# Kernel tuning notes

Measured on AMD Instinct MI355X. Metric: run time of the kernel, lower is better.

## Reference

```python
import jax, jax.numpy as jnp
import numpy as np

B, LX, LY, D = 8, 2048, 2048, 256

def setup_inputs() -> dict:
    key = jax.random.key(0)
    k1, k2, k3, k4 = jax.random.split(key, 4)
    x = jax.random.normal(k1, (B, LX, D), dtype=jnp.float32)
    y = jax.random.normal(k2, (B, LY, D), dtype=jnp.float32)
    y_mask = jax.random.randint(k3, (B, LY), 0, 2).astype(jnp.bool_)
    W = jax.random.normal(k4, (D, D), dtype=jnp.float32) * (1.0 / np.sqrt(D))
    b = jnp.zeros((D,), dtype=jnp.float32)
    return {"x": x, "y": y, "y_mask": y_mask, "W": W, "b": b}

def reference(x, y, y_mask, W, b):
    # shared linear + relu projection (torch Linear: x @ W.T + b)
    x_proj = jax.nn.relu(jnp.einsum('bld,ed->ble', x, W) + b)  # [B,LX,D]
    y_proj = jax.nn.relu(jnp.einsum('bld,ed->ble', y, W) + b)  # [B,LY,D]
    scores = jnp.einsum('bxd,byd->bxy', x_proj, y_proj)        # [B,LX,LY]
    scores = jnp.where(y_mask[:, None, :], -jnp.inf, scores)
    alpha = jax.nn.softmax(scores, axis=-1)                    # [B,LX,LY]
    return jnp.einsum('bxy,byd->bxd', alpha, y)                # [B,LX,D]
```

## Files before the change

### kernel.cpp

```cpp
#include <hip/hip_runtime.h>

typedef __attribute__((ext_vector_type(8))) short short8;
typedef _Float16 half8 __attribute__((ext_vector_type(8)));
typedef __attribute__((ext_vector_type(4))) float f32x4;
typedef __attribute__((ext_vector_type(4))) unsigned int uint4v;
typedef __attribute__((ext_vector_type(2))) unsigned int uint2v;

#define B_   8
#define LX_  2048
#define LY_  2048
#define D_   256
#define NROW (B_ * LX_)

__device__ __forceinline__ unsigned short f2bf(float f) {
  unsigned u = __builtin_bit_cast(unsigned, f);
  u += 0x7FFF + ((u >> 16) & 1);
  return (unsigned short)(u >> 16);
}
__device__ __forceinline__ float bf2f(unsigned short h) {
  unsigned u = ((unsigned)h) << 16;
  return __builtin_bit_cast(float, u);
}

__global__ __launch_bounds__(256) void wsplit_kernel(
    const float* __restrict__ W, unsigned short* __restrict__ Whi,
    unsigned short* __restrict__ Wlo) {
  int i = blockIdx.x * 256 + threadIdx.x;
  float w = W[i];
  unsigned short hi = f2bf(w);
  Whi[i] = hi;
  Wlo[i] = f2bf(w - bf2f(hi));
}

__global__ __launch_bounds__(256) void scan_kernel(
    const int* __restrict__ MASK, int* __restrict__ CIDX, int* __restrict__ Lc) {
  __shared__ int s[256];
  __shared__ int base_s[256];
  int b = blockIdx.x, t = threadIdx.x;
  int f[8];
  int cnt = 0;
  for (int k = 0; k < 8; ++k) {
    f[k] = (MASK[b * 2048 + t * 8 + k] == 0) ? 1 : 0;
    cnt += f[k];
  }
  s[t] = cnt;
  __syncthreads();
  if (t == 0) {
    int run = 0;
    for (int i = 0; i < 256; ++i) { int v = s[i]; base_s[i] = run; run += v; }
    Lc[b] = run;
  }
  __syncthreads();
  int off = base_s[t];
  for (int k = 0; k < 8; ++k)
    if (f[k]) CIDX[b * 2048 + (off++)] = t * 8 + k;
}

__global__ __launch_bounds__(256, 2) void proj_kernel(
    const float* __restrict__ X, const float* __restrict__ Y,
    const float* __restrict__ bias,
    const unsigned short* __restrict__ Whi, const unsigned short* __restrict__ Wlo,
    _Float16* __restrict__ XP, _Float16* __restrict__ YP) {
  __shared__ unsigned short Ah[64][40], Al[64][40];
  __shared__ unsigned short Bh[256][40], Bl[256][40];

  int t = threadIdx.x;
  int lane = t & 63, wave = t >> 6;
  int q = lane >> 4, n15 = lane & 15;

  const float* src;
  _Float16* dst;
  int m0;
  if (blockIdx.x < 256) { src = X; dst = XP; m0 = blockIdx.x * 64; }
  else                  { src = Y; dst = YP; m0 = (blockIdx.x - 256) * 64; }

  f32x4 acc[4][4];
  for (int mt = 0; mt < 4; ++mt)
    for (int nt = 0; nt < 4; ++nt) acc[mt][nt] = (f32x4){0.f, 0.f, 0.f, 0.f};

  int arow = t >> 2;
  int aseg = t & 3;
  int erow = t >> 2, ec = t & 3;

  for (int kc = 0; kc < 8; ++kc) {
    __syncthreads();
    for (int i = 0; i < 2; ++i) {
      int seg = aseg + i * 4;
      f32x4 f = *(const f32x4*)(src + (size_t)(m0 + arow) * D_ + kc * 32 + seg * 4);
      unsigned short h[4], l[4];
      for (int j = 0; j < 4; ++j) {
        h[j] = f2bf(f[j]);
        l[j] = f2bf(f[j] - bf2f(h[j]));
      }
      uint2v vh = {(unsigned)h[0] | ((unsigned)h[1] << 16),
                   (unsigned)h[2] | ((unsigned)h[3] << 16)};
      uint2v vl = {(unsigned)l[0] | ((unsigned)l[1] << 16),
                   (unsigned)l[2] | ((unsigned)l[3] << 16)};
      *(uint2v*)&Ah[arow][seg * 4] = vh;
      *(uint2v*)&Al[arow][seg * 4] = vl;
    }
    for (int pass = 0; pass < 4; ++pass) {
      int e = pass * 64 + erow;
      uint4v vh = *(const uint4v*)(Whi + (size_t)e * D_ + kc * 32 + ec * 8);
      uint4v vl = *(const uint4v*)(Wlo + (size_t)e * D_ + kc * 32 + ec * 8);
      *(uint4v*)&Bh[e][ec * 8] = vh;
      *(uint4v*)&Bl[e][ec * 8] = vl;
    }
    __syncthreads();
    short8 afh[4], afl[4], bfh[4], bfl[4];
    for (int mt = 0; mt < 4; ++mt) {
      afh[mt] = *(const short8*)&Ah[mt * 16 + n15][q * 8];
      afl[mt] = *(const short8*)&Al[mt * 16 + n15][q * 8];
    }
    for (int nt = 0; nt < 4; ++nt) {
      bfh[nt] = *(const short8*)&Bh[wave * 64 + nt * 16 + n15][q * 8];
      bfl[nt] = *(const short8*)&Bl[wave * 64 + nt * 16 + n15][q * 8];
    }
    for (int mt = 0; mt < 4; ++mt)
      for (int nt = 0; nt < 4; ++nt) {
        acc[mt][nt] = __builtin_amdgcn_mfma_f32_16x16x32_bf16(afh[mt], bfh[nt], acc[mt][nt], 0, 0, 0);
        acc[mt][nt] = __builtin_amdgcn_mfma_f32_16x16x32_bf16(afl[mt], bfh[nt], acc[mt][nt], 0, 0, 0);
        acc[mt][nt] = __builtin_amdgcn_mfma_f32_16x16x32_bf16(afh[mt], bfl[nt], acc[mt][nt], 0, 0, 0);
      }
  }

  for (int nt = 0; nt < 4; ++nt) {
    int e = wave * 64 + nt * 16 + n15;
    float bv = bias[e];
    for (int mt = 0; mt < 4; ++mt)
      for (int r = 0; r < 4; ++r) {
        float v = acc[mt][nt][r] + bv;
        v = v > 0.f ? v : 0.f;
        dst[(size_t)(m0 + mt * 16 + q * 4 + r) * D_ + e] = (_Float16)v;
      }
  }
}

__global__ __launch_bounds__(256) void gather_rows_kernel(
    const _Float16* __restrict__ YP, const int* __restrict__ CIDX,
    const int* __restrict__ Lc, _Float16* __restrict__ YPc) {
  int g = blockIdx.x * 256 + threadIdx.x;
  int rowid = g >> 5, seg = g & 31;
  int b = rowid >> 11, j = rowid & 2047;
  int idx = (j < Lc[b]) ? CIDX[b * 2048 + j] : 0;
  uint4v v = *(const uint4v*)(YP + ((size_t)(b << 11) + idx) * D_ + seg * 8);
  *(uint4v*)(YPc + (size_t)rowid * D_ + seg * 8) = v;
}

__global__ __launch_bounds__(256) void gatherT_kernel(
    const float* __restrict__ Y, const int* __restrict__ CIDX,
    const int* __restrict__ Lc, _Float16* __restrict__ YTc) {
  __shared__ _Float16 tile[64][72];
  int id = blockIdx.x;
  int db = id & 3, nb = (id >> 2) & 31, b = id >> 7;
  int t = threadIdx.x;
  int nl = t >> 2, ds = t & 3;
  int j = nb * 64 + nl;
  int idx = (j < Lc[b]) ? CIDX[b * 2048 + j] : 0;
  const float* src = Y + (size_t)(b * LY_ + idx) * D_ + db * 64 + ds * 16;
  for (int i = 0; i < 4; ++i) {
    f32x4 f = *(const f32x4*)(src + i * 4);
    for (int k = 0; k < 4; ++k) tile[ds * 16 + i * 4 + k][nl] = (_Float16)f[k];
  }
  __syncthreads();
  int dl = t >> 2, nsub = t & 3;
  uint4v v0 = *(const uint4v*)&tile[dl][nsub * 16];
  uint4v v1 = *(const uint4v*)&tile[dl][nsub * 16 + 8];
  _Float16* dst = YTc + (size_t)(b * D_ + db * 64 + dl) * LY_ + nb * 64 + nsub * 16;
  *(uint4v*)(dst) = v0;
  *(uint4v*)(dst + 8) = v1;
}

__global__ __launch_bounds__(256, 2) void flash_kernel(
    const _Float16* __restrict__ XP, const _Float16* __restrict__ YPc,
    const _Float16* __restrict__ YTc, const int* __restrict__ Lc,
    _Float16* __restrict__ PO, float* __restrict__ Pm, float* __restrict__ Pl) {
  __shared__ _Float16 yp_t[32][264];
  __shared__ _Float16 yT_t[256][40];
  __shared__ _Float16 pbuf[4][16][40];

  int t = threadIdx.x;
  int lane = t & 63, wave = t >> 6;
  int q = lane >> 4, n15 = lane & 15;
  int half = blockIdx.x & 1;
  int xb = (blockIdx.x >> 1) & 31;
  int b = blockIdx.x >> 6;
  int row0 = xb * 64 + wave * 16;

  int lc = Lc[b];
  int T  = (lc + 31) >> 5;
  int T0 = (T + 1) >> 1;
  int tstart = half ? T0 : 0;
  int tend   = half ? T  : T0;

  half8 a[8];
  const _Float16* xrow = XP + (size_t)(b * LX_ + row0 + n15) * D_ + q * 8;
  for (int kk = 0; kk < 8; ++kk) a[kk] = *(const half8*)(xrow + kk * 32);

  half8 lones;
  for (int j = 0; j < 8; ++j) lones[j] = (n15 == 0) ? (_Float16)1 : (_Float16)0;

  float m_r[4];
  for (int r = 0; r < 4; ++r) m_r[r] = -1e30f;
  f32x4 lacc = {0.f, 0.f, 0.f, 0.f};
  f32x4 oacc[16];
  for (int dt = 0; dt < 16; ++dt) oacc[dt] = (f32x4){0.f, 0.f, 0.f, 0.f};

  const _Float16* ypb = YPc + (size_t)b * LY_ * D_;
  const _Float16* yTb = YTc + (size_t)b * D_ * LY_;

  uint4v pr[8];
#define PREFETCH(tt)                                                          \
  {                                                                           \
    int y0p = (tt) * 32;                                                      \
    for (int i = 0; i < 4; ++i) {                                             \
      int c = t + i * 256;                                                    \
      pr[i] = *(const uint4v*)(ypb + (size_t)(y0p + (c >> 5)) * D_ + (c & 31) * 8); \
    }                                                                         \
    for (int i = 0; i < 4; ++i) {                                             \
      int c = t + i * 256;                                                    \
      pr[4 + i] = *(const uint4v*)(yTb + (size_t)(c >> 2) * LY_ + y0p + (c & 3) * 8); \
    }                                                                         \
  }

  if (tstart < tend) PREFETCH(tstart);

  for (int tt = tstart; tt < tend; ++tt) {
    int y0 = tt * 32;
    __syncthreads();
    for (int i = 0; i < 4; ++i) {
      int c = t + i * 256;
      *(uint4v*)&yp_t[c >> 5][(c & 31) * 8] = pr[i];
    }
    for (int i = 0; i < 4; ++i) {
      int c = t + i * 256;
      *(uint4v*)&yT_t[c >> 2][(c & 3) * 8] = pr[4 + i];
    }
    if (tt + 1 < tend) PREFETCH(tt + 1);
    __syncthreads();

    f32x4 S0 = {0.f, 0.f, 0.f, 0.f}, S1 = {0.f, 0.f, 0.f, 0.f};
    for (int kk = 0; kk < 8; ++kk) {
      half8 b0 = *(const half8*)&yp_t[n15][kk * 32 + q * 8];
      S0 = __builtin_amdgcn_mfma_f32_16x16x32_f16(a[kk], b0, S0, 0, 0, 0);
    }
    for (int kk = 0; kk < 8; ++kk) {
      half8 b1 = *(const half8*)&yp_t[16 + n15][kk * 32 + q * 8];
      S1 = __builtin_amdgcn_mfma_f32_16x16x32_f16(a[kk], b1, S1, 0, 0, 0);
    }
    bool mk0 = (y0 + n15) >= lc;
    bool mk1 = (y0 + 16 + n15) >= lc;

    float al[4];
    _Float16 ph0[4], ph1[4];
    bool need = false;
    for (int r = 0; r < 4; ++r) {
      float s0 = mk0 ? -1e30f : S0[r];
      float s1 = mk1 ? -1e30f : S1[r];
      float tm = fmaxf(s0, s1);
      tm = fmaxf(tm, __shfl_xor(tm, 1));
      tm = fmaxf(tm, __shfl_xor(tm, 2));
      tm = fmaxf(tm, __shfl_xor(tm, 4));
      tm = fmaxf(tm, __shfl_xor(tm, 8));
      float mn = fmaxf(m_r[r], tm);
      al[r] = __expf(m_r[r] - mn);
      m_r[r] = mn;
      ph0[r] = (_Float16)__expf(s0 - mn);
      ph1[r] = (_Float16)__expf(s1 - mn);
      need = need || (al[r] != 1.0f);
    }
    if (__ballot(need)) {
      for (int dt = 0; dt < 16; ++dt)
        for (int r = 0; r < 4; ++r) oacc[dt][r] *= al[r];
      for (int r = 0; r < 4; ++r) lacc[r] *= al[r];
    }
    for (int r = 0; r < 4; ++r) {
      pbuf[wave][q * 4 + r][n15] = ph0[r];
      pbuf[wave][q * 4 + r][16 + n15] = ph1[r];
    }
    half8 pa = *(const half8*)&pbuf[wave][n15][q * 8];
    lacc = __builtin_amdgcn_mfma_f32_16x16x32_f16(pa, lones, lacc, 0, 0, 0);
    for (int dt = 0; dt < 16; ++dt) {
      half8 bb = *(const half8*)&yT_t[dt * 16 + n15][q * 8];
      oacc[dt] = __builtin_amdgcn_mfma_f32_16x16x32_f16(pa, bb, oacc[dt], 0, 0, 0);
    }
  }
#undef PREFETCH

  size_t prow = (size_t)(half * B_ + b) * LX_ + row0;
  _Float16* po = PO + prow * D_;
  for (int dt = 0; dt < 16; ++dt)
    for (int r = 0; r < 4; ++r)
      po[(size_t)(q * 4 + r) * D_ + dt * 16 + n15] = (_Float16)oacc[dt][r];
  if (n15 == 0) {
    for (int r = 0; r < 4; ++r) {
      Pm[prow + q * 4 + r] = m_r[r];
      Pl[prow + q * 4 + r] = lacc[r];
    }
  }
}

__global__ __launch_bounds__(256) void merge_kernel(
    const _Float16* __restrict__ PO, const float* __restrict__ Pm,
    const float* __restrict__ Pl, float* __restrict__ OUT) {
  int c = blockIdx.x * 256 + threadIdx.x;
  int row = c >> 5, seg = c & 31;
  float m0 = Pm[row], m1 = Pm[NROW + row];
  float l0 = Pl[row], l1 = Pl[NROW + row];
  float m = fmaxf(m0, m1);
  float w0 = __expf(m0 - m), w1 = __expf(m1 - m);
  float inv = 1.0f / (l0 * w0 + l1 * w1);
  const _Float16* p0 = PO + (size_t)row * D_ + seg * 8;
  const _Float16* p1 = p0 + (size_t)NROW * D_;
  half8 a = *(const half8*)p0;
  half8 bsec = *(const half8*)p1;
  float* o = OUT + (size_t)row * D_ + seg * 8;
  f32x4 o0, o1;
  for (int j = 0; j < 4; ++j) o0[j] = ((float)a[j] * w0 + (float)bsec[j] * w1) * inv;
  for (int j = 0; j < 4; ++j) o1[j] = ((float)a[4 + j] * w0 + (float)bsec[4 + j] * w1) * inv;
  *(f32x4*)o = o0;
  *(f32x4*)(o + 4) = o1;
}

extern "C" void kernel_launch(void* const* d_in, const int* in_sizes, int n_in,
                              void* d_out, int out_size, void* d_ws, size_t ws_size,
                              hipStream_t stream) {
  const float* x     = (const float*)d_in[0];
  const float* y     = (const float*)d_in[1];
  const int*   ymask = (const int*)  d_in[2];
  const float* W     = (const float*)d_in[3];
  const float* bias  = (const float*)d_in[4];
  float* out = (float*)d_out;

  char* ws = (char*)d_ws;
  unsigned short* Whi = (unsigned short*)(ws);
  unsigned short* Wlo = (unsigned short*)(ws + 131072);
  _Float16* XP  = (_Float16*)(ws + 262144);
  _Float16* YP  = (_Float16*)(ws + 262144 + 8388608);
  _Float16* YPc = (_Float16*)(ws + 262144 + 2 * 8388608);
  _Float16* YTc = (_Float16*)(ws + 262144 + 3 * 8388608);
  _Float16* PO  = (_Float16*)(ws + 262144 + 4 * 8388608);
  char* tail = ws + 262144 + 4 * 8388608 + 16777216;
  float* Pm   = (float*)(tail);
  float* Pl   = (float*)(tail + 131072);
  int*   CIDX = (int*)  (tail + 262144);
  int*   Lc   = (int*)  (tail + 262144 + 65536);

  wsplit_kernel<<<256, 256, 0, stream>>>(W, Whi, Wlo);
  scan_kernel<<<8, 256, 0, stream>>>(ymask, CIDX, Lc);
  proj_kernel<<<512, 256, 0, stream>>>(x, y, bias, Whi, Wlo, XP, YP);
  gather_rows_kernel<<<2048, 256, 0, stream>>>(YP, CIDX, Lc, YPc);
  gatherT_kernel<<<1024, 256, 0, stream>>>(y, CIDX, Lc, YTc);
  flash_kernel<<<512, 256, 0, stream>>>(XP, YPc, YTc, Lc, PO, Pm, Pl);
  merge_kernel<<<2048, 256, 0, stream>>>(PO, Pm, Pl, out);
}
```

Before: 161.9 us.

## Scatter projected Y rows directly into compacted buffer, prefetch proj loads

The projection kernel now writes each unmasked Y row straight to its compacted position through a per-row position map built in the scan, which removes the separate gather_rows pass and the intermediate full YP buffer. The scan becomes a parallel Hillis-Steele prefix sum, and a small kernel zeroes the padding rows in the compacted buffer. The proj kernel also register-prefetches the next K-chunk of X and W before the MFMA work, and gatherT skips tiles entirely beyond the padded compacted length. In exchange there is one extra small launch and scattered row stores in the projection epilogue.

```diff
diff --git a/kernel.cpp b/kernel.cpp
--- a/kernel.cpp
+++ b/kernel.cpp
@@ -33,9 +33,9 @@
 }
 
 __global__ __launch_bounds__(256) void scan_kernel(
-    const int* __restrict__ MASK, int* __restrict__ CIDX, int* __restrict__ Lc) {
+    const int* __restrict__ MASK, int* __restrict__ CIDX,
+    int* __restrict__ CPOS, int* __restrict__ Lc) {
   __shared__ int s[256];
-  __shared__ int base_s[256];
   int b = blockIdx.x, t = threadIdx.x;
   int f[8];
   int cnt = 0;
@@ -45,22 +45,45 @@
   }
   s[t] = cnt;
   __syncthreads();
-  if (t == 0) {
-    int run = 0;
-    for (int i = 0; i < 256; ++i) { int v = s[i]; base_s[i] = run; run += v; }
-    Lc[b] = run;
-  }
-  __syncthreads();
-  int off = base_s[t];
-  for (int k = 0; k < 8; ++k)
-    if (f[k]) CIDX[b * 2048 + (off++)] = t * 8 + k;
+  for (int off = 1; off < 256; off <<= 1) {
+    int v = (t >= off) ? s[t - off] : 0;
+    __syncthreads();
+    s[t] += v;
+    __syncthreads();
+  }
+  if (t == 255) Lc[b] = s[255];
+  int off = s[t] - cnt;
+  for (int k = 0; k < 8; ++k) {
+    int j = t * 8 + k;
+    if (f[k]) {
+      CIDX[b * 2048 + off] = j;
+      CPOS[b * 2048 + j] = b * 2048 + off;
+      ++off;
+    } else {
+      CPOS[b * 2048 + j] = -1;
+    }
+  }
+}
+
+__global__ __launch_bounds__(256) void zero_tail_kernel(
+    const int* __restrict__ Lc, _Float16* __restrict__ YPc) {
+  int b = blockIdx.x;
+  int lc = Lc[b];
+  int end = (lc + 31) & ~31;
+  int total = (end - lc) * 32;
+  for (int c = threadIdx.x; c < total; c += 256) {
+    int rr = c >> 5, seg = c & 31;
+    uint4v z = {0, 0, 0, 0};
+    *(uint4v*)(YPc + (size_t)(b * 2048 + lc + rr) * D_ + seg * 8) = z;
+  }
 }
 
 __global__ __launch_bounds__(256, 2) void proj_kernel(
     const float* __restrict__ X, const float* __restrict__ Y,
     const float* __restrict__ bias,
     const unsigned short* __restrict__ Whi, const unsigned short* __restrict__ Wlo,
-    _Float16* __restrict__ XP, _Float16* __restrict__ YP) {
+    const int* __restrict__ CPOS,
+    _Float16* __restrict__ XP, _Float16* __restrict__ YPc) {
   __shared__ unsigned short Ah[64][40], Al[64][40];
   __shared__ unsigned short Bh[256][40], Bl[256][40];
 
@@ -68,25 +91,38 @@
   int lane = t & 63, wave = t >> 6;
   int q = lane >> 4, n15 = lane & 15;
 
-  const float* src;
-  _Float16* dst;
-  int m0;
-  if (blockIdx.x < 256) { src = X; dst = XP; m0 = blockIdx.x * 64; }
-  else                  { src = Y; dst = YP; m0 = (blockIdx.x - 256) * 64; }
+  bool isX = blockIdx.x < 256;
+  const float* src = isX ? X : Y;
+  int m0 = (isX ? blockIdx.x : (blockIdx.x - 256)) * 64;
 
   f32x4 acc[4][4];
   for (int mt = 0; mt < 4; ++mt)
     for (int nt = 0; nt < 4; ++nt) acc[mt][nt] = (f32x4){0.f, 0.f, 0.f, 0.f};
 
-  int arow = t >> 2;
-  int aseg = t & 3;
+  int arow = t >> 2, aseg = t & 3;
   int erow = t >> 2, ec = t & 3;
+
+  f32x4 pa[2];
+  uint4v pbh[4], pbl[4];
+#define PROJ_PF(kc)                                                            \
+  {                                                                            \
+    for (int i = 0; i < 2; ++i)                                                \
+      pa[i] = *(const f32x4*)(src + (size_t)(m0 + arow) * D_ + (kc) * 32 +     \
+                              (aseg + i * 4) * 4);                             \
+    for (int p = 0; p < 4; ++p) {                                              \
+      int e = p * 64 + erow;                                                   \
+      pbh[p] = *(const uint4v*)(Whi + (size_t)e * D_ + (kc) * 32 + ec * 8);    \
+      pbl[p] = *(const uint4v*)(Wlo + (size_t)e * D_ + (kc) * 32 + ec * 8);    \
+    }                                                                          \
+  }
+
+  PROJ_PF(0);
 
   for (int kc = 0; kc < 8; ++kc) {
     __syncthreads();
     for (int i = 0; i < 2; ++i) {
       int seg = aseg + i * 4;
-      f32x4 f = *(const f32x4*)(src + (size_t)(m0 + arow) * D_ + kc * 32 + seg * 4);
+      f32x4 f = pa[i];
       unsigned short h[4], l[4];
       for (int j = 0; j < 4; ++j) {
         h[j] = f2bf(f[j]);
@@ -99,14 +135,14 @@
       *(uint2v*)&Ah[arow][seg * 4] = vh;
       *(uint2v*)&Al[arow][seg * 4] = vl;
     }
-    for (int pass = 0; pass < 4; ++pass) {
-      int e = pass * 64 + erow;
-      uint4v vh = *(const uint4v*)(Whi + (size_t)e * D_ + kc * 32 + ec * 8);
-      uint4v vl = *(const uint4v*)(Wlo + (size_t)e * D_ + kc * 32 + ec * 8);
-      *(uint4v*)&Bh[e][ec * 8] = vh;
-      *(uint4v*)&Bl[e][ec * 8] = vl;
-    }
-    __syncthreads();
+    for (int p = 0; p < 4; ++p) {
+      int e = p * 64 + erow;
+      *(uint4v*)&Bh[e][ec * 8] = pbh[p];
+      *(uint4v*)&Bl[e][ec * 8] = pbl[p];
+    }
+    if (kc < 7) PROJ_PF(kc + 1);
+    __syncthreads();
+
     short8 afh[4], afl[4], bfh[4], bfl[4];
     for (int mt = 0; mt < 4; ++mt) {
       afh[mt] = *(const short8*)&Ah[mt * 16 + n15][q * 8];
@@ -123,28 +159,28 @@
         acc[mt][nt] = __builtin_amdgcn_mfma_f32_16x16x32_bf16(afh[mt], bfl[nt], acc[mt][nt], 0, 0, 0);
       }
   }
-
+#undef PROJ_PF
+
+  int drow[16];
+  for (int mt = 0; mt < 4; ++mt)
+    for (int r = 0; r < 4; ++r) {
+      int row = m0 + mt * 16 + q * 4 + r;
+      drow[mt * 4 + r] = isX ? row : CPOS[row];
+    }
+  _Float16* dst = isX ? XP : YPc;
   for (int nt = 0; nt < 4; ++nt) {
     int e = wave * 64 + nt * 16 + n15;
     float bv = bias[e];
     for (int mt = 0; mt < 4; ++mt)
       for (int r = 0; r < 4; ++r) {
-        float v = acc[mt][nt][r] + bv;
-        v = v > 0.f ? v : 0.f;
-        dst[(size_t)(m0 + mt * 16 + q * 4 + r) * D_ + e] = (_Float16)v;
+        int dr = drow[mt * 4 + r];
+        if (dr >= 0) {
+          float v = acc[mt][nt][r] + bv;
+          v = v > 0.f ? v : 0.f;
+          dst[(size_t)dr * D_ + e] = (_Float16)v;
+        }
       }
   }
-}
-
-__global__ __launch_bounds__(256) void gather_rows_kernel(
-    const _Float16* __restrict__ YP, const int* __restrict__ CIDX,
-    const int* __restrict__ Lc, _Float16* __restrict__ YPc) {
-  int g = blockIdx.x * 256 + threadIdx.x;
-  int rowid = g >> 5, seg = g & 31;
-  int b = rowid >> 11, j = rowid & 2047;
-  int idx = (j < Lc[b]) ? CIDX[b * 2048 + j] : 0;
-  uint4v v = *(const uint4v*)(YP + ((size_t)(b << 11) + idx) * D_ + seg * 8);
-  *(uint4v*)(YPc + (size_t)rowid * D_ + seg * 8) = v;
 }
 
 __global__ __launch_bounds__(256) void gatherT_kernel(
@@ -153,10 +189,13 @@
   __shared__ _Float16 tile[64][72];
   int id = blockIdx.x;
   int db = id & 3, nb = (id >> 2) & 31, b = id >> 7;
+  int lc = Lc[b];
+  int end = (lc + 31) & ~31;
+  if (nb * 64 >= end) return;
   int t = threadIdx.x;
   int nl = t >> 2, ds = t & 3;
   int j = nb * 64 + nl;
-  int idx = (j < Lc[b]) ? CIDX[b * 2048 + j] : 0;
+  int idx = (j < lc) ? CIDX[b * 2048 + j] : 0;
   const float* src = Y + (size_t)(b * LY_ + idx) * D_ + db * 64 + ds * 16;
   for (int i = 0; i < 4; ++i) {
     f32x4 f = *(const f32x4*)(src + i * 4);
@@ -336,20 +375,20 @@
   unsigned short* Whi = (unsigned short*)(ws);
   unsigned short* Wlo = (unsigned short*)(ws + 131072);
   _Float16* XP  = (_Float16*)(ws + 262144);
-  _Float16* YP  = (_Float16*)(ws + 262144 + 8388608);
-  _Float16* YPc = (_Float16*)(ws + 262144 + 2 * 8388608);
-  _Float16* YTc = (_Float16*)(ws + 262144 + 3 * 8388608);
-  _Float16* PO  = (_Float16*)(ws + 262144 + 4 * 8388608);
-  char* tail = ws + 262144 + 4 * 8388608 + 16777216;
+  _Float16* YPc = (_Float16*)(ws + 262144 + 8388608);
+  _Float16* YTc = (_Float16*)(ws + 262144 + 2 * 8388608);
+  _Float16* PO  = (_Float16*)(ws + 262144 + 3 * 8388608);
+  char* tail = ws + 262144 + 3 * 8388608 + 16777216;
   float* Pm   = (float*)(tail);
   float* Pl   = (float*)(tail + 131072);
   int*   CIDX = (int*)  (tail + 262144);
-  int*   Lc   = (int*)  (tail + 262144 + 65536);
+  int*   CPOS = (int*)  (tail + 262144 + 65536);
+  int*   Lc   = (int*)  (tail + 262144 + 131072);
 
   wsplit_kernel<<<256, 256, 0, stream>>>(W, Whi, Wlo);
-  scan_kernel<<<8, 256, 0, stream>>>(ymask, CIDX, Lc);
-  proj_kernel<<<512, 256, 0, stream>>>(x, y, bias, Whi, Wlo, XP, YP);
-  gather_rows_kernel<<<2048, 256, 0, stream>>>(YP, CIDX, Lc, YPc);
+  scan_kernel<<<8, 256, 0, stream>>>(ymask, CIDX, CPOS, Lc);
+  zero_tail_kernel<<<8, 256, 0, stream>>>(Lc, YPc);
+  proj_kernel<<<512, 256, 0, stream>>>(x, y, bias, Whi, Wlo, CPOS, XP, YPc);
   gatherT_kernel<<<1024, 256, 0, stream>>>(y, CIDX, Lc, YTc);
   flash_kernel<<<512, 256, 0, stream>>>(XP, YPc, YTc, Lc, PO, Pm, Pl);
   merge_kernel<<<2048, 256, 0, stream>>>(PO, Pm, Pl, out);
```

Result: slower. 166.6 us (+2.9%).
